# Kernel tuning notes

Hardware: AMD Instinct MI355X
Metric: run time of the kernel (lower is better)

The kernel has to match this reference:

```python
import jax, jax.numpy as jnp
import numpy as np


def setup_inputs() -> dict:
    key = jax.random.key(0)
    N, C, H, W, D = 4, 128, 48, 48, 48
    x = jax.random.normal(key, (N, C, H, W, D), dtype=jnp.float32)
    return {"x": x}


def reference(x) -> jnp.ndarray:
    # Channel self-attention over flattened spatial dims.
    N, C, H, W, D = x.shape
    q = x.reshape(N, C, -1)                      # [N, C, S]
    # energy[n, i, j] = <channel i, channel j>
    energy = jnp.einsum('ncs,nms->ncm', q, q)    # [N, C, C]
    # max-subtract trick (note: softmax of (max - energy), NOT energy - max)
    energy_new = jnp.max(energy, axis=-1, keepdims=True) - energy
    attention = jax.nn.softmax(energy_new, axis=-1)  # [N, C, C]
    out = jnp.einsum('ncm,nms->ncs', attention, q)   # [N, C, S]
    return out.reshape(N, C, H, W, D)
```

## Files before the change

### kernel.cpp

```cpp
#include <hip/hip_runtime.h>
#include <math.h>


static constexpr int CN = 128;
static constexpr int SN = 110592;
static constexpr int NB = 4;

static constexpr int GB = 108;
static constexpr int GSL = SN / GB;
static constexpr int GCH = GSL / 64;

static constexpr int PB = 432;
static constexpr int PCH = 4;

typedef float  f32x4  __attribute__((ext_vector_type(4)));
typedef short  bf16x8 __attribute__((ext_vector_type(8)));
typedef unsigned short u16x8 __attribute__((ext_vector_type(8)));
typedef unsigned short u16x4 __attribute__((ext_vector_type(4)));

__device__ __forceinline__ unsigned int splitpack(float v) {
    unsigned int u = __float_as_uint(v);
    unsigned int h = (u + 0x7fffu + ((u >> 16) & 1u)) >> 16;
    float lf = v - __uint_as_float(h << 16);
    unsigned int ul = __float_as_uint(lf);
    unsigned int l = (ul + 0x7fffu + ((ul >> 16) & 1u)) >> 16;
    return (l << 16) | (h & 0xffffu);
}
__device__ __forceinline__ unsigned short f2bh(float v) {
    unsigned int u = __float_as_uint(v);
    return (unsigned short)((u + 0x7fffu + ((u >> 16) & 1u)) >> 16);
}

__device__ __forceinline__ bf16x8 ldsfrag(const unsigned short* base, int row, int kbyte, int pitchB) {
    const char* p = reinterpret_cast<const char*>(base) + row * pitchB + (kbyte ^ ((row & 7) << 4));
    return *reinterpret_cast<const bf16x8*>(p);
}
__device__ __forceinline__ f32x4 mm(bf16x8 a, bf16x8 b, f32x4 c) {
    return __builtin_amdgcn_mfma_f32_16x16x32_bf16(a, b, c, 0, 0, 0);
}

template <bool ATOMIC>
__global__ __launch_bounds__(512, 2) void gram_mfma(const float* __restrict__ x,
                                                    float* __restrict__ dst) {
    __shared__ __align__(16) unsigned short lh[2][CN * 64];
    __shared__ __align__(16) unsigned short ll[2][CN * 64];
    const int bx = blockIdx.x, n = blockIdx.y;
    const int tid = threadIdx.x;
    const int lane = tid & 63;
    const int w = tid >> 6;
    const int wr = w >> 2, wc = w & 3;
    const int ra = lane & 15, kg = lane >> 4;

    const int c  = tid >> 2;
    const int ks = (tid & 3) << 4;
    const float* gq = x + (size_t)n * CN * SN + (size_t)c * SN + bx * GSL;

    f32x4 acc[4][2];
#pragma unroll
    for (int a = 0; a < 4; ++a)
#pragma unroll
        for (int b = 0; b < 2; ++b) acc[a][b] = (f32x4){0.f, 0.f, 0.f, 0.f};

    float4 st[4];
    auto load_chunk = [&](int t) {
        const float4* p = reinterpret_cast<const float4*>(gq + t * 64 + ks);
        st[0] = p[0]; st[1] = p[1]; st[2] = p[2]; st[3] = p[3];
    };

    auto stage = [&](int buf) {
        u16x8 ha, hb, la, lb;
        unsigned int p;
#define CV8(hv, lv, i, val) { p = splitpack(val); hv[i] = (unsigned short)(p & 0xffffu); lv[i] = (unsigned short)(p >> 16); }
        CV8(ha, la, 0, st[0].x) CV8(ha, la, 1, st[0].y) CV8(ha, la, 2, st[0].z) CV8(ha, la, 3, st[0].w)
        CV8(ha, la, 4, st[1].x) CV8(ha, la, 5, st[1].y) CV8(ha, la, 6, st[1].z) CV8(ha, la, 7, st[1].w)
        CV8(hb, lb, 0, st[2].x) CV8(hb, lb, 1, st[2].y) CV8(hb, lb, 2, st[2].z) CV8(hb, lb, 3, st[2].w)
        CV8(hb, lb, 4, st[3].x) CV8(hb, lb, 5, st[3].y) CV8(hb, lb, 6, st[3].z) CV8(hb, lb, 7, st[3].w)
#undef CV8
        char* ph = reinterpret_cast<char*>(lh[buf]) + c * 128;
        char* pl = reinterpret_cast<char*>(ll[buf]) + c * 128;
        const int sw = (c & 7) << 4;
        const int k2 = ks * 2;
        *reinterpret_cast<u16x8*>(ph + (k2 ^ sw))        = ha;
        *reinterpret_cast<u16x8*>(ph + ((k2 + 16) ^ sw)) = hb;
        *reinterpret_cast<u16x8*>(pl + (k2 ^ sw))        = la;
        *reinterpret_cast<u16x8*>(pl + ((k2 + 16) ^ sw)) = lb;
    };

    auto compute = [&](int buf) {
        const unsigned short* LH = lh[buf];
        const unsigned short* LL = ll[buf];
#pragma unroll
        for (int kk = 0; kk < 2; ++kk) {
            const int kb = kk * 64 + (kg << 4);
            bf16x8 ah[4], al[4], bh[2], bl[2];
#pragma unroll
            for (int it = 0; it < 4; ++it) {
                const int row = wr * 64 + it * 16 + ra;
                ah[it] = ldsfrag(LH, row, kb, 128);
                al[it] = ldsfrag(LL, row, kb, 128);
            }
#pragma unroll
            for (int jt = 0; jt < 2; ++jt) {
                const int row = wc * 32 + jt * 16 + ra;
                bh[jt] = ldsfrag(LH, row, kb, 128);
                bl[jt] = ldsfrag(LL, row, kb, 128);
            }
#pragma unroll
            for (int it = 0; it < 4; ++it)
#pragma unroll
                for (int jt = 0; jt < 2; ++jt) {
                    acc[it][jt] = mm(ah[it], bh[jt], acc[it][jt]);
                    acc[it][jt] = mm(ah[it], bl[jt], acc[it][jt]);
                    acc[it][jt] = mm(al[it], bh[jt], acc[it][jt]);
                }
        }
    };

    load_chunk(0);
    for (int t = 0; t < GCH; ++t) {
        stage(t & 1);
        if (t < GCH - 1) load_chunk(t + 1);
        __syncthreads();
        compute(t & 1);
    }

    const int q4 = kg << 2;
    if (!ATOMIC) {
        float* P = dst + (size_t)(n * GB + bx) * (CN * CN);
#pragma unroll
        for (int it = 0; it < 4; ++it)
#pragma unroll
            for (int jt = 0; jt < 2; ++jt)
#pragma unroll
                for (int q = 0; q < 4; ++q)
                    __builtin_nontemporal_store(acc[it][jt][q],
                        &P[(wr * 64 + it * 16 + q4 + q) * CN + wc * 32 + jt * 16 + ra]);
    } else {
        float* E = dst + (size_t)n * CN * CN;
#pragma unroll
        for (int it = 0; it < 4; ++it)
#pragma unroll
            for (int jt = 0; jt < 2; ++jt)
#pragma unroll
                for (int q = 0; q < 4; ++q)
                    atomicAdd(&E[(wr * 64 + it * 16 + q4 + q) * CN + wc * 32 + jt * 16 + ra], acc[it][jt][q]);
    }
}

template <bool REDUCE>
__global__ void finish_kernel(const float* __restrict__ src,
                              unsigned short* __restrict__ att_h) {
    const int i = blockIdx.x, n = blockIdx.y, l = threadIdx.x;
    float e0, e1;
    if (REDUCE) {
        const float* p = src + (size_t)n * GB * (CN * CN) + i * CN;
        e0 = 0.f; e1 = 0.f;
#pragma unroll 4
        for (int k = 0; k < GB; ++k) {
            e0 += __builtin_nontemporal_load(&p[(size_t)k * (CN * CN) + l]);
            e1 += __builtin_nontemporal_load(&p[(size_t)k * (CN * CN) + l + 64]);
        }
    } else {
        const float* E = src + ((size_t)n * CN + i) * CN;
        e0 = E[l]; e1 = E[l + 64];
    }
    float m = fminf(e0, e1);
#pragma unroll
    for (int off = 32; off > 0; off >>= 1) m = fminf(m, __shfl_xor(m, off));
    const float p0 = expf(m - e0);
    const float p1 = expf(m - e1);
    float s = p0 + p1;
#pragma unroll
    for (int off = 32; off > 0; off >>= 1) s += __shfl_xor(s, off);
    const float inv = 1.f / s;
    const size_t o = ((size_t)n * CN + i) * CN;
    att_h[o + l]      = f2bh(p0 * inv);
    att_h[o + l + 64] = f2bh(p1 * inv);
}

__global__ __launch_bounds__(512, 4) void pv_mfma(const float* __restrict__ x,
                                                  const unsigned short* __restrict__ att_h,
                                                  float* __restrict__ out) {
    __shared__ __align__(16) unsigned short qh[2][64 * CN];
    const int bx = blockIdx.x, n = blockIdx.y;
    const int tid = threadIdx.x;
    const int lane = tid & 63;
    const int w = tid >> 6;
    const int ra = lane & 15, kg = lane >> 4;

    bf16x8 a_h[4];
    {
        const size_t rowoff = ((size_t)n * CN + w * 16 + ra) * CN + kg * 8;
        const unsigned short* Ah = att_h + rowoff;
#pragma unroll
        for (int kk = 0; kk < 4; ++kk)
            a_h[kk] = *reinterpret_cast<const bf16x8*>(Ah + kk * 32);
    }

    const int j0 = (tid >> 4) * 4;
    const int s0 = (tid & 15) * 4;
    const float* gx = x + (size_t)n * CN * SN;
    const int sbase = bx * (PCH * 64);

    f32x4 st[4];
    auto load_chunk = [&](int sb) {
#pragma unroll
        for (int r = 0; r < 4; ++r)
            st[r] = *reinterpret_cast<const f32x4*>(gx + (size_t)(j0 + r) * SN + sb + s0);
    };

    auto stage = [&](int buf) {
        char* base = reinterpret_cast<char*>(qh[buf]);
#pragma unroll
        for (int r = 0; r < 4; ++r) {
            u16x4 hv;
            hv[0] = f2bh(st[0][r]);
            hv[1] = f2bh(st[1][r]);
            hv[2] = f2bh(st[2][r]);
            hv[3] = f2bh(st[3][r]);
            const int s = s0 + r;
            const int off = s * 256 + ((j0 * 2) ^ ((s & 7) << 4));
            *reinterpret_cast<u16x4*>(base + off) = hv;
        }
    };

    auto compute = [&](int buf, int sb) {
        const unsigned short* Q = qh[buf];
#pragma unroll
        for (int stile = 0; stile < 4; ++stile) {
            f32x4 acc = (f32x4){0.f, 0.f, 0.f, 0.f};
            const int srow = stile * 16 + ra;
#pragma unroll
            for (int kk = 0; kk < 4; ++kk) {
                const int kb = kk * 64 + (kg << 4);
                bf16x8 bh = ldsfrag(Q, srow, kb, 256);
                acc = mm(a_h[kk], bh, acc);
            }
            float* o = out + ((size_t)n * CN + w * 16 + (kg << 2)) * SN + sb + stile * 16 + ra;
#pragma unroll
            for (int q = 0; q < 4; ++q)
                __builtin_nontemporal_store(acc[q], o + (size_t)q * SN);
        }
    };

    load_chunk(sbase);
    for (int t = 0; t < PCH; ++t) {
        stage(t & 1);
        if (t < PCH - 1) load_chunk(sbase + (t + 1) * 64);
        __syncthreads();
        compute(t & 1, sbase + t * 64);
    }
}

extern "C" void kernel_launch(void* const* d_in, const int* in_sizes, int n_in,
                              void* d_out, int out_size, void* d_ws, size_t ws_size,
                              hipStream_t stream) {
    (void)in_sizes; (void)n_in; (void)out_size;
    const float* x = (const float*)d_in[0];
    float* out = (float*)d_out;

    float* energy = (float*)d_ws;
    unsigned short* att_h = (unsigned short*)(energy + (size_t)NB * CN * CN);
    float* part = (float*)(att_h + (size_t)NB * CN * CN);
    const size_t need =
        (size_t)NB * CN * CN * sizeof(float) +
        (size_t)NB * CN * CN * sizeof(unsigned short) +
        (size_t)NB * GB * CN * CN * sizeof(float);

    if (ws_size >= need) {
        gram_mfma<false><<<dim3(GB, NB), 512, 0, stream>>>(x, part);
        finish_kernel<true><<<dim3(CN, NB), 64, 0, stream>>>(part, att_h);
    } else {
        hipMemsetAsync(energy, 0, (size_t)NB * CN * CN * sizeof(float), stream);
        gram_mfma<true><<<dim3(GB, NB), 512, 0, stream>>>(x, energy);
        finish_kernel<false><<<dim3(CN, NB), 64, 0, stream>>>(energy, att_h);
    }
    pv_mfma<<<dim3(PB, NB), 512, 0, stream>>>(x, att_h, out);
}
```

Measured before the change: 154.4 us.

## Fuse gram, softmax and PV stages into one cooperative kernel with grid syncs

Replaces the three-kernel pipeline with a single cooperative kernel of 256 blocks. Each block computes a partial Gram over its spatial slice, then after a grid sync two waves per block reduce partials and apply the softmax. After a second grid sync each block runs the PV product over its own slice, whose data may still be in L2. The aim is to remove launch gaps and shrink the partial-sum reduction traffic by cutting gram blocks from 108 to 64. The cost is much less parallelism in the PV phase (256 blocks instead of 1728), grid-sync overhead, and a fallback path if the cooperative launch fails.

```diff
diff --git a/kernel.cpp b/kernel.cpp
--- a/kernel.cpp
+++ b/kernel.cpp
@@ -1,12 +1,15 @@
 #include <hip/hip_runtime.h>
+#include <hip/hip_cooperative_groups.h>
 #include <math.h>
+
+namespace cg = cooperative_groups;
 
 
 static constexpr int CN = 128;
 static constexpr int SN = 110592;
 static constexpr int NB = 4;
 
-static constexpr int GB = 108;
+static constexpr int GB = 64;
 static constexpr int GSL = SN / GB;
 static constexpr int GCH = GSL / 64;
 
@@ -37,6 +40,201 @@
 }
 __device__ __forceinline__ f32x4 mm(bf16x8 a, bf16x8 b, f32x4 c) {
     return __builtin_amdgcn_mfma_f32_16x16x32_bf16(a, b, c, 0, 0, 0);
+}
+
+__global__ __launch_bounds__(512, 2) void fused_cse(const float* __restrict__ x,
+                                                    float* __restrict__ part,
+                                                    unsigned short* __restrict__ att_h,
+                                                    float* __restrict__ out) {
+    __shared__ __align__(16) unsigned short lh[2][CN * 64];
+    __shared__ __align__(16) unsigned short ll[2][CN * 64];
+    const int blk = blockIdx.x;
+    const int n  = blk >> 6;
+    const int bx = blk & 63;
+    const int tid = threadIdx.x;
+    const int lane = tid & 63;
+    const int w = tid >> 6;
+    const int ra = lane & 15, kg = lane >> 4;
+
+    {
+        const int wr = w >> 2, wc = w & 3;
+        const int c  = tid >> 2;
+        const int ks = (tid & 3) << 4;
+        const float* gq = x + (size_t)n * CN * SN + (size_t)c * SN + bx * GSL;
+
+        f32x4 acc[4][2];
+#pragma unroll
+        for (int a = 0; a < 4; ++a)
+#pragma unroll
+            for (int b = 0; b < 2; ++b) acc[a][b] = (f32x4){0.f, 0.f, 0.f, 0.f};
+
+        float4 st[4];
+        auto load_chunk = [&](int t) {
+            const float4* p = reinterpret_cast<const float4*>(gq + t * 64 + ks);
+            st[0] = p[0]; st[1] = p[1]; st[2] = p[2]; st[3] = p[3];
+        };
+
+        auto stage = [&](int buf) {
+            u16x8 ha, hb, la, lb;
+            unsigned int p;
+#define CV8(hv, lv, i, val) { p = splitpack(val); hv[i] = (unsigned short)(p & 0xffffu); lv[i] = (unsigned short)(p >> 16); }
+            CV8(ha, la, 0, st[0].x) CV8(ha, la, 1, st[0].y) CV8(ha, la, 2, st[0].z) CV8(ha, la, 3, st[0].w)
+            CV8(ha, la, 4, st[1].x) CV8(ha, la, 5, st[1].y) CV8(ha, la, 6, st[1].z) CV8(ha, la, 7, st[1].w)
+            CV8(hb, lb, 0, st[2].x) CV8(hb, lb, 1, st[2].y) CV8(hb, lb, 2, st[2].z) CV8(hb, lb, 3, st[2].w)
+            CV8(hb, lb, 4, st[3].x) CV8(hb, lb, 5, st[3].y) CV8(hb, lb, 6, st[3].z) CV8(hb, lb, 7, st[3].w)
+#undef CV8
+            char* ph = reinterpret_cast<char*>(lh[buf]) + c * 128;
+            char* pl = reinterpret_cast<char*>(ll[buf]) + c * 128;
+            const int sw = (c & 7) << 4;
+            const int k2 = ks * 2;
+            *reinterpret_cast<u16x8*>(ph + (k2 ^ sw))        = ha;
+            *reinterpret_cast<u16x8*>(ph + ((k2 + 16) ^ sw)) = hb;
+            *reinterpret_cast<u16x8*>(pl + (k2 ^ sw))        = la;
+            *reinterpret_cast<u16x8*>(pl + ((k2 + 16) ^ sw)) = lb;
+        };
+
+        auto compute = [&](int buf) {
+            const unsigned short* LH = lh[buf];
+            const unsigned short* LL = ll[buf];
+#pragma unroll
+            for (int kk = 0; kk < 2; ++kk) {
+                const int kb = kk * 64 + (kg << 4);
+                bf16x8 ah[4], al[4], bh[2], bl[2];
+#pragma unroll
+                for (int it = 0; it < 4; ++it) {
+                    const int row = wr * 64 + it * 16 + ra;
+                    ah[it] = ldsfrag(LH, row, kb, 128);
+                    al[it] = ldsfrag(LL, row, kb, 128);
+                }
+#pragma unroll
+                for (int jt = 0; jt < 2; ++jt) {
+                    const int row = wc * 32 + jt * 16 + ra;
+                    bh[jt] = ldsfrag(LH, row, kb, 128);
+                    bl[jt] = ldsfrag(LL, row, kb, 128);
+                }
+#pragma unroll
+                for (int it = 0; it < 4; ++it)
+#pragma unroll
+                    for (int jt = 0; jt < 2; ++jt) {
+                        acc[it][jt] = mm(ah[it], bh[jt], acc[it][jt]);
+                        acc[it][jt] = mm(ah[it], bl[jt], acc[it][jt]);
+                        acc[it][jt] = mm(al[it], bh[jt], acc[it][jt]);
+                    }
+            }
+        };
+
+        load_chunk(0);
+        for (int t = 0; t < GCH; ++t) {
+            stage(t & 1);
+            if (t < GCH - 1) load_chunk(t + 1);
+            __syncthreads();
+            compute(t & 1);
+        }
+
+        const int q4 = kg << 2;
+        float* P = part + (size_t)(n * GB + bx) * (CN * CN);
+#pragma unroll
+        for (int it = 0; it < 4; ++it)
+#pragma unroll
+            for (int jt = 0; jt < 2; ++jt)
+#pragma unroll
+                for (int q = 0; q < 4; ++q)
+                    __builtin_nontemporal_store(acc[it][jt][q],
+                        &P[(wr * 64 + it * 16 + q4 + q) * CN + wc * 32 + jt * 16 + ra]);
+    }
+
+    cg::this_grid().sync();
+
+    if (w < 2) {
+        const int r = blk * 2 + w;
+        const int fn = r >> 7, fi = r & 127;
+        const float* p = part + (size_t)fn * GB * (CN * CN) + fi * CN;
+        float e0 = 0.f, e1 = 0.f;
+#pragma unroll 8
+        for (int k = 0; k < GB; ++k) {
+            e0 += __builtin_nontemporal_load(&p[(size_t)k * (CN * CN) + lane]);
+            e1 += __builtin_nontemporal_load(&p[(size_t)k * (CN * CN) + lane + 64]);
+        }
+        float m = fminf(e0, e1);
+#pragma unroll
+        for (int off = 32; off > 0; off >>= 1) m = fminf(m, __shfl_xor(m, off));
+        const float p0 = expf(m - e0);
+        const float p1 = expf(m - e1);
+        float s = p0 + p1;
+#pragma unroll
+        for (int off = 32; off > 0; off >>= 1) s += __shfl_xor(s, off);
+        const float inv = 1.f / s;
+        const size_t o = ((size_t)fn * CN + fi) * CN;
+        att_h[o + lane]      = f2bh(p0 * inv);
+        att_h[o + lane + 64] = f2bh(p1 * inv);
+    }
+
+    cg::this_grid().sync();
+
+    {
+        bf16x8 a_h[4];
+        {
+            const size_t rowoff = ((size_t)n * CN + w * 16 + ra) * CN + kg * 8;
+            const unsigned short* Ah = att_h + rowoff;
+#pragma unroll
+            for (int kk = 0; kk < 4; ++kk)
+                a_h[kk] = *reinterpret_cast<const bf16x8*>(Ah + kk * 32);
+        }
+
+        const int j0 = (tid >> 4) * 4;
+        const int s0 = (tid & 15) * 4;
+        const float* gx = x + (size_t)n * CN * SN;
+        const int sbase = bx * GSL;
+
+        f32x4 st[4];
+        auto pv_load = [&](int sb) {
+#pragma unroll
+            for (int r = 0; r < 4; ++r)
+                st[r] = *reinterpret_cast<const f32x4*>(gx + (size_t)(j0 + r) * SN + sb + s0);
+        };
+
+        auto pv_stage = [&](int buf) {
+            char* base = reinterpret_cast<char*>(lh[buf]);
+#pragma unroll
+            for (int r = 0; r < 4; ++r) {
+                u16x4 hv;
+                hv[0] = f2bh(st[0][r]);
+                hv[1] = f2bh(st[1][r]);
+                hv[2] = f2bh(st[2][r]);
+                hv[3] = f2bh(st[3][r]);
+                const int s = s0 + r;
+                const int off = s * 256 + ((j0 * 2) ^ ((s & 7) << 4));
+                *reinterpret_cast<u16x4*>(base + off) = hv;
+            }
+        };
+
+        auto pv_compute = [&](int buf, int sb) {
+            const unsigned short* Q = lh[buf];
+#pragma unroll
+            for (int stile = 0; stile < 4; ++stile) {
+                f32x4 acc = (f32x4){0.f, 0.f, 0.f, 0.f};
+                const int srow = stile * 16 + ra;
+#pragma unroll
+                for (int kk = 0; kk < 4; ++kk) {
+                    const int kb = kk * 64 + (kg << 4);
+                    bf16x8 bh = ldsfrag(Q, srow, kb, 256);
+                    acc = mm(a_h[kk], bh, acc);
+                }
+                float* o = out + ((size_t)n * CN + w * 16 + (kg << 2)) * SN + sb + stile * 16 + ra;
+#pragma unroll
+                for (int q = 0; q < 4; ++q)
+                    __builtin_nontemporal_store(acc[q], o + (size_t)q * SN);
+            }
+        };
+
+        pv_load(sbase);
+        for (int t = 0; t < GCH; ++t) {
+            pv_stage(t & 1);
+            if (t < GCH - 1) pv_load(sbase + (t + 1) * 64);
+            __syncthreads();
+            pv_compute(t & 1, sbase + t * 64);
+        }
+    }
 }
 
 template <bool ATOMIC>
@@ -50,7 +248,6 @@
     const int w = tid >> 6;
     const int wr = w >> 2, wc = w & 3;
     const int ra = lane & 15, kg = lane >> 4;
-
     const int c  = tid >> 2;
     const int ks = (tid & 3) << 4;
     const float* gq = x + (size_t)n * CN * SN + (size_t)c * SN + bx * GSL;
@@ -66,7 +263,6 @@
         const float4* p = reinterpret_cast<const float4*>(gq + t * 64 + ks);
         st[0] = p[0]; st[1] = p[1]; st[2] = p[2]; st[3] = p[3];
     };
-
     auto stage = [&](int buf) {
         u16x8 ha, hb, la, lb;
         unsigned int p;
@@ -85,7 +281,6 @@
         *reinterpret_cast<u16x8*>(pl + (k2 ^ sw))        = la;
         *reinterpret_cast<u16x8*>(pl + ((k2 + 16) ^ sw)) = lb;
     };
-
     auto compute = [&](int buf) {
         const unsigned short* LH = lh[buf];
         const unsigned short* LL = ll[buf];
@@ -155,7 +350,7 @@
     if (REDUCE) {
         const float* p = src + (size_t)n * GB * (CN * CN) + i * CN;
         e0 = 0.f; e1 = 0.f;
-#pragma unroll 4
+#pragma unroll 8
         for (int k = 0; k < GB; ++k) {
             e0 += __builtin_nontemporal_load(&p[(size_t)k * (CN * CN) + l]);
             e1 += __builtin_nontemporal_load(&p[(size_t)k * (CN * CN) + l + 64]);
@@ -208,7 +403,6 @@
         for (int r = 0; r < 4; ++r)
             st[r] = *reinterpret_cast<const f32x4*>(gx + (size_t)(j0 + r) * SN + sb + s0);
     };
-
     auto stage = [&](int buf) {
         char* base = reinterpret_cast<char*>(qh[buf]);
 #pragma unroll
@@ -223,7 +417,6 @@
             *reinterpret_cast<u16x4*>(base + off) = hv;
         }
     };
-
     auto compute = [&](int buf, int sb) {
         const unsigned short* Q = qh[buf];
 #pragma unroll
@@ -268,12 +461,22 @@
         (size_t)NB * GB * CN * CN * sizeof(float);
 
     if (ws_size >= need) {
+        const float* xa = x;
+        float* pa = part;
+        unsigned short* aa = att_h;
+        float* oa = out;
+        void* args[] = {(void*)&xa, (void*)&pa, (void*)&aa, (void*)&oa};
+        hipError_t err = hipLaunchCooperativeKernel(
+            (const void*)fused_cse, dim3(GB * NB), dim3(512), args, 0, stream);
+        if (err == hipSuccess) return;
+
         gram_mfma<false><<<dim3(GB, NB), 512, 0, stream>>>(x, part);
         finish_kernel<true><<<dim3(CN, NB), 64, 0, stream>>>(part, att_h);
+        pv_mfma<<<dim3(PB, NB), 512, 0, stream>>>(x, att_h, out);
     } else {
         hipMemsetAsync(energy, 0, (size_t)NB * CN * CN * sizeof(float), stream);
         gram_mfma<true><<<dim3(GB, NB), 512, 0, stream>>>(x, energy);
         finish_kernel<false><<<dim3(CN, NB), 64, 0, stream>>>(energy, att_h);
-    }
-    pv_mfma<<<dim3(PB, NB), 512, 0, stream>>>(x, att_h, out);
-}
+        pv_mfma<<<dim3(PB, NB), 512, 0, stream>>>(x, att_h, out);
+    }
+}
```

After: 212.2 us. 1.37x slower.
